# Optimization experiments

Measured on AMD Instinct MI355X. Metric: run time of the kernel, lower is better.

Reference implementation:

```python
import jax, jax.numpy as jnp
import numpy as np

N = 10000      # atoms
E = 160000     # edges (avg degree 16)
G = 20         # graphs
Z = 10         # num_elements
K = 64         # hidden scalar channels (hidden_irreps multiplicity)
NB = 8         # num_bessel
H = 64         # radial MLP width
LMAX = 3
LM = (LMAX + 1) ** 2   # 16 spherical-harmonic components
M = 16         # MLP_irreps width for final nonlinear readout
R_MAX = 5.0
AVG_NEIGH = 16.0
LS = np.array([l for l in range(LMAX + 1) for _ in range(2 * l + 1)])  # l index of each lm slot


def _sph(u):
    # real spherical harmonics up to l=3, 'component' normalization, on unit vectors u [E,3]
    x, y, z = u[:, 0], u[:, 1], u[:, 2]
    s3, s5, s15, s7 = 3.0 ** 0.5, 5.0 ** 0.5, 15.0 ** 0.5, 7.0 ** 0.5
    c31, c32, c33 = (21.0 / 8.0) ** 0.5, 105.0 ** 0.5, (35.0 / 8.0) ** 0.5
    Y = [jnp.ones_like(x),
         s3 * x, s3 * y, s3 * z,
         s15 * x * y, s15 * y * z, 0.5 * s5 * (3 * z * z - 1.0), s15 * x * z, 0.5 * s15 * (x * x - y * y),
         c33 * y * (3 * x * x - y * y), c32 * x * y * z, c31 * y * (5 * z * z - 1.0),
         0.5 * s7 * z * (5 * z * z - 3.0),
         c31 * x * (5 * z * z - 1.0), 0.5 * c32 * z * (x * x - y * y), c33 * x * (x * x - 3 * y * y)]
    return jnp.stack(Y, axis=-1)


def _radial(r):
    # Bessel radial basis with p=5 polynomial cutoff envelope
    u = r / R_MAX
    n = jnp.arange(1, NB + 1, dtype=r.dtype)
    bess = (2.0 / R_MAX) ** 0.5 * jnp.sin(n[None, :] * jnp.pi * u[:, None]) / r[:, None]
    env = jnp.where(u < 1.0, 1.0 - 21.0 * u ** 5 + 35.0 * u ** 6 - 15.0 * u ** 7, 0.0)
    return bess * env[:, None]


def _forward(node_attrs, positions, atomic_energies, W_embed, radial_W0, radial_W1, radial_W2, radial_W3, W_mix, Wz, W_out, w_read1, W_r1, w_r2, edge_index, batch):
    sender, receiver = edge_index[0], edge_index[1]
    vec = positions[receiver] - positions[sender]          # edge gather
    r = jnp.sqrt(jnp.sum(vec * vec, axis=-1) + 1e-12)
    Y = _sph(vec / r[:, None])                             # [E, 16]
    edge_feats = _radial(r)                                # [E, NB]
    node_e0 = node_attrs @ atomic_energies                 # [N]
    feats = node_attrs @ W_embed                           # node embedding [N, K]
    node_en = node_e0
    for t in range(2):  # num_interactions
        # radial MLP -> per-(channel,l) tensor-product weights
        h = edge_feats
        for W in (radial_W0[t], radial_W1[t], radial_W2[t]):
            h = jax.nn.silu(h @ W)
        Rw = (h @ radial_W3[t]).reshape(-1, K, LMAX + 1)[:, :, LS]   # [E, K, 16]
        # channelwise tensor product: sender feats x SH x radial weights
        msg = feats[sender][:, :, None] * Rw * Y[:, None, :]         # [E, K, 16]
        A = jax.ops.segment_sum(msg, receiver, num_segments=node_attrs.shape[0]) / AVG_NEIGH
        A = jnp.einsum('nkm,mkc->ncm', A, W_mix[t][LS])              # per-l linear channel mixing
        # equivariant product basis (correlation 3) -> invariant contractions with element-dep weights
        s1 = A[:, :, 0]
        inv2 = jnp.sum(A * A, axis=-1)
        b = (node_attrs @ Wz[t, 0]) * s1 + (node_attrs @ Wz[t, 1]) * inv2 + (node_attrs @ Wz[t, 2]) * (s1 * inv2)
        feats = b @ W_out[t]
        if t == 0:
            node_en = node_en + feats @ w_read1              # linear readout
        else:
            node_en = node_en + jax.nn.silu(feats @ W_r1) @ w_r2  # nonlinear readout
    return jax.ops.segment_sum(node_en, batch, num_segments=G)      # per-graph energies [G]


def setup_inputs():
    key = jax.random.key(0)
    ks = jax.random.split(key, 16)
    gn = lambda k, shape, fan: jax.random.normal(k, shape, dtype=jnp.float32) / (fan ** 0.5)
    species = jax.random.randint(ks[0], (N,), 0, Z)
    return {
        'node_attrs': jax.nn.one_hot(species, Z, dtype=jnp.float32),
        'positions': jax.random.normal(ks[1], (N, 3), dtype=jnp.float32) * 3.0,
        'edge_index': jax.random.randint(ks[2], (2, E), 0, N),
        'batch': jnp.sort(jax.random.randint(ks[3], (N,), 0, G)),
        'atomic_energies': jax.random.normal(ks[4], (Z,), dtype=jnp.float32),
        'W_embed': gn(ks[5], (Z, K), Z),
        'radial_W0': gn(ks[6], (2, NB, H), NB),
        'radial_W1': gn(ks[7], (2, H, H), H),
        'radial_W2': gn(ks[8], (2, H, H), H),
        'radial_W3': gn(ks[9], (2, H, K * (LMAX + 1)), H),
        'W_mix': gn(ks[10], (2, LMAX + 1, K, K), K),
        'Wz': gn(ks[11], (2, 3, Z, K), Z),
        'W_out': gn(ks[12], (2, K, K), K),
        'w_read1': gn(ks[13], (K,), K),
        'W_r1': gn(ks[14], (K, M), K),
        'w_r2': gn(ks[15], (M,), M),
    }


def reference(node_attrs, positions, edge_index, batch, atomic_energies, W_embed, radial_W0, radial_W1, radial_W2, radial_W3, W_mix, Wz, W_out, w_read1, W_r1, w_r2):
    return _forward(node_attrs, positions, atomic_energies, W_embed, radial_W0, radial_W1, radial_W2, radial_W3, W_mix, Wz, W_out, w_read1, W_r1, w_r2, edge_index, batch)
```

## Files before the change

kernel.cpp:

```cpp
#include <hip/hip_runtime.h>
#include <hip/hip_bf16.h>
#include <math.h>

#define NN 10000
#define NE 160000
#define NG 20
#define NZ 10
#define INV_AVG 0.0625f

typedef __attribute__((ext_vector_type(8))) short bf16x8;
typedef __attribute__((ext_vector_type(4))) float f32x4;
typedef __attribute__((ext_vector_type(4))) unsigned short u16x4;
typedef __attribute__((ext_vector_type(8))) unsigned short u16x8;

__device__ __forceinline__ float silu(float x) { return x / (1.0f + __expf(-x)); }

__device__ __forceinline__ unsigned short f2b(float f) {
    union { float f; unsigned u; } v; v.f = f;
    unsigned r = v.u + 0x7FFF + ((v.u >> 16) & 1);
    return (unsigned short)(r >> 16);
}
__device__ __forceinline__ float b2f(unsigned short h) {
    union { unsigned u; float f; } v; v.u = ((unsigned)h) << 16; return v.f;
}

__global__ __launch_bounds__(256) void node_init(
    const float* __restrict__ attrs, const float* __restrict__ W_embed,
    const float* __restrict__ ae,
    float* __restrict__ feats, float* __restrict__ node_en)
{
    int gid = blockIdx.x * blockDim.x + threadIdx.x;
    if (gid >= NN * 64) return;
    int n = gid >> 6, k = gid & 63;
    float acc = 0.f;
#pragma unroll
    for (int z = 0; z < NZ; ++z) acc += attrs[n * NZ + z] * W_embed[z * 64 + k];
    feats[gid] = acc;
    if (k == 0) {
        float e0 = 0.f;
#pragma unroll
        for (int z = 0; z < NZ; ++z) e0 += attrs[n * NZ + z] * ae[z];
        node_en[n] = e0;
    }
}

__global__ __launch_bounds__(256) void csr_count(const int* __restrict__ ei, int* __restrict__ cnt)
{
    int e = blockIdx.x * 256 + threadIdx.x;
    if (e < NE) atomicAdd(&cnt[ei[NE + e]], 1);
}

__global__ __launch_bounds__(1024) void csr_scan(const int* __restrict__ cnt, int* __restrict__ row)
{
    __shared__ int part[1024];
    const int tid = threadIdx.x;
    const int base = tid * 10;
    int loc[10];
    int s = 0;
#pragma unroll
    for (int q = 0; q < 10; ++q) {
        int idx = base + q;
        int v = (idx < NN) ? cnt[idx] : 0;
        loc[q] = s; s += v;
    }
    part[tid] = s;
    __syncthreads();
    for (int off = 1; off < 1024; off <<= 1) {
        int v = (tid >= off) ? part[tid - off] : 0;
        __syncthreads();
        part[tid] += v;
        __syncthreads();
    }
    int pre = (tid > 0) ? part[tid - 1] : 0;
#pragma unroll
    for (int q = 0; q < 10; ++q) {
        int idx = base + q;
        if (idx < NN) row[idx] = pre + loc[q];
    }
    if (tid == 1023) row[NN] = part[1023];
}

__global__ __launch_bounds__(256) void csr_scatter(
    const int* __restrict__ ei, const int* __restrict__ row,
    int* __restrict__ cur, int* __restrict__ perm)
{
    int e = blockIdx.x * 256 + threadIdx.x;
    if (e < NE) {
        int r = ei[NE + e];
        int p = atomicAdd(&cur[r], 1);
        perm[row[r] + p] = e;
    }
}

__global__ __launch_bounds__(256) void w_prep(
    const float* __restrict__ rW0, const float* __restrict__ rW1,
    const float* __restrict__ rW2, const float* __restrict__ rW3,
    const float* __restrict__ Wmix,
    unsigned short* __restrict__ w0f, unsigned short* __restrict__ w1f,
// ... 12 lines not shown
        int fidx = x >> 9, l = (x >> 3) & 63, j = x & 7;
        int kt = fidx >> 2, nt = fidx & 3;
        int k = kt * 32 + (l >> 4) * 8 + j, c = nt * 16 + (l & 15);
        w1f[x0] = f2b(rW1[t * 4096 + k * 64 + c]);
    } else if (g < 36864) {
        int x0 = g - 20480;
        int t = x0 >> 13, x = x0 & 8191;
        int fidx = x >> 9, l = (x >> 3) & 63, j = x & 7;
        int kt = fidx >> 2, nt = fidx & 3;
        int k = kt * 32 + (l >> 4) * 8 + j, c = nt * 16 + (l & 15);
        w2f[x0] = f2b(rW2[t * 4096 + k * 64 + c]);
    } else if (g < 69632) {
        int x0 = g - 36864;
        int t = x0 >> 14, x = x0 & 16383;
        int fidx = x >> 9, l = (x >> 3) & 63, j = x & 7;
        int kt = fidx >> 4, nt = fidx & 15;
        int k = kt * 32 + (l >> 4) * 8 + j, c = nt * 16 + (l & 15);
        w3f[x0] = f2b(rW3[t * 16384 + k * 256 + c]);
    } else if (g < 102400) {
        int x0 = g - 69632;
        int t = x0 >> 14;
        int x = x0 & 16383;
        int l = x >> 12;
        int xx = x & 4095;
        int f = xx >> 9, ll = (xx >> 3) & 63, j = xx & 7;
        int kt = f >> 2, ct = f & 3;
        int k = kt * 32 + (ll >> 4) * 8 + j, c = ct * 16 + (ll & 15);
        wmixf[x0] = f2b(Wmix[t * 16384 + l * 4096 + k * 64 + c]);
    }
}

__global__ __launch_bounds__(256) void edge_geom(
    const int* __restrict__ ei, const float* __restrict__ pos,
    const int* __restrict__ perm,
    unsigned short* __restrict__ ybg, unsigned short* __restrict__ ebg,
    int* __restrict__ snd_p)
{
    const int g = blockIdx.x * 256 + threadIdx.x;
    const int e = perm[g];
    const int snd = ei[e], rcv = ei[NE + e];
    snd_p[g] = snd;
    const float dx = pos[rcv * 3 + 0] - pos[snd * 3 + 0];
    const float dy = pos[rcv * 3 + 1] - pos[snd * 3 + 1];
    const float dz = pos[rcv * 3 + 2] - pos[snd * 3 + 2];
    const float r = sqrtf(dx * dx + dy * dy + dz * dz + 1e-12f);
    const float ir = 1.0f / r;
    const float x = dx * ir, y = dy * ir, z = dz * ir;
    const float xx = x * x, yy = y * y, zz = z * z;

    u16x8 ylo, yhi;
    ylo[0] = f2b(1.0f);
    ylo[1] = f2b(1.73205081f * x);
    ylo[2] = f2b(1.73205081f * y);
    ylo[3] = f2b(1.73205081f * z);
    ylo[4] = f2b(3.87298335f * x * y);
    ylo[5] = f2b(3.87298335f * y * z);
    ylo[6] = f2b(1.11803399f * (3.0f * zz - 1.0f));
    ylo[7] = f2b(3.87298335f * x * z);
    yhi[0] = f2b(1.93649167f * (xx - yy));
    yhi[1] = f2b(2.09165007f * y * (3.0f * xx - yy));
    yhi[2] = f2b(10.2469508f * x * y * z);
    yhi[3] = f2b(1.62018517f * y * (5.0f * zz - 1.0f));
    yhi[4] = f2b(1.32287566f * z * (5.0f * zz - 3.0f));
    yhi[5] = f2b(1.62018517f * x * (5.0f * zz - 1.0f));
    yhi[6] = f2b(5.12347538f * z * (xx - yy));
    yhi[7] = f2b(2.09165007f * x * (xx - 3.0f * yy));
    *(u16x8*)&ybg[(size_t)g * 16] = ylo;
    *(u16x8*)&ybg[(size_t)g * 16 + 8] = yhi;

    const float u = r * 0.2f;
    float env = 0.0f;
    if (u < 1.0f) {
        const float u2 = u * u, u5 = u2 * u2 * u;
        env = 1.0f - 21.0f * u5 + 35.0f * u5 * u - 15.0f * u5 * u2;
    }
    const float cb = 0.632455532f * ir * env;
    const float pu = 3.14159265358979f * u;
    u16x8 eb;
#pragma unroll
    for (int i = 0; i < 8; ++i) eb[i] = f2b(cb * __sinf((float)(i + 1) * pu));
    *(u16x8*)&ebg[(size_t)g * 8] = eb;
}

__global__ __launch_bounds__(256) void radial_fused(
    const unsigned short* __restrict__ ebg,
    const unsigned short* __restrict__ w0f,
    const unsigned short* __restrict__ w1f,
    const unsigned short* __restrict__ w2f,
    const unsigned short* __restrict__ w3f,
    unsigned short* __restrict__ rwb)
{
    __shared__ unsigned short sP[4][2][16 * 72];
    const int w = threadIdx.x >> 6, lane = threadIdx.x & 63;
    const int tIdx = blockIdx.x * 4 + w;
    const int lg = lane >> 4, e16 = lane & 15;
    unsigned short* ping = &sP[w][0][0];
    unsigned short* pong = &sP[w][1][0];

    const size_t g0 = (size_t)tIdx * 16;
    f32x4 c[4];

    bf16x8 a1 = {0, 0, 0, 0, 0, 0, 0, 0};
    if (lg == 0) a1 = *(const bf16x8*)&ebg[(g0 + e16) * 8];
#pragma unroll
    for (int nt = 0; nt < 4; ++nt) {
        const bf16x8 b = *(const bf16x8*)&w0f[nt * 512 + lane * 8];
        c[nt] = __builtin_amdgcn_mfma_f32_16x16x32_bf16(a1, b, (f32x4){0.f, 0.f, 0.f, 0.f}, 0, 0, 0);
    }
#pragma unroll
    for (int nt = 0; nt < 4; ++nt)
#pragma unroll
        for (int jj = 0; jj < 4; ++jj)
            ping[(lg * 4 + jj) * 72 + nt * 16 + e16] = f2b(silu(c[nt][jj]));

    {
        const bf16x8 ak0 = *(const bf16x8*)&ping[e16 * 72 + lg * 8];
        const bf16x8 ak1 = *(const bf16x8*)&ping[e16 * 72 + 32 + lg * 8];
#pragma unroll
        for (int nt = 0; nt < 4; ++nt) {
            const bf16x8 b0 = *(const bf16x8*)&w1f[nt * 512 + lane * 8];
            const bf16x8 b1 = *(const bf16x8*)&w1f[(4 + nt) * 512 + lane * 8];
            f32x4 acc = __builtin_amdgcn_mfma_f32_16x16x32_bf16(ak0, b0, (f32x4){0.f, 0.f, 0.f, 0.f}, 0, 0, 0);
            c[nt] = __builtin_amdgcn_mfma_f32_16x16x32_bf16(ak1, b1, acc, 0, 0, 0);
        }
    }
#pragma unroll
    for (int nt = 0; nt < 4; ++nt)
#pragma unroll
        for (int jj = 0; jj < 4; ++jj)
            pong[(lg * 4 + jj) * 72 + nt * 16 + e16] = f2b(silu(c[nt][jj]));

    {
        const bf16x8 ak0 = *(const bf16x8*)&pong[e16 * 72 + lg * 8];
        const bf16x8 ak1 = *(const bf16x8*)&pong[e16 * 72 + 32 + lg * 8];
#pragma unroll
        for (int nt = 0; nt < 4; ++nt) {
            const bf16x8 b0 = *(const bf16x8*)&w2f[nt * 512 + lane * 8];
            const bf16x8 b1 = *(const bf16x8*)&w2f[(4 + nt) * 512 + lane * 8];
            f32x4 acc = __builtin_amdgcn_mfma_f32_16x16x32_bf16(ak0, b0, (f32x4){0.f, 0.f, 0.f, 0.f}, 0, 0, 0);
            c[nt] = __builtin_amdgcn_mfma_f32_16x16x32_bf16(ak1, b1, acc, 0, 0, 0);
        }
    }
#pragma unroll
    for (int nt = 0; nt < 4; ++nt)
#pragma unroll
        for (int jj = 0; jj < 4; ++jj)
            ping[(lg * 4 + jj) * 72 + nt * 16 + e16] = f2b(silu(c[nt][jj]));

    const bf16x8 h0 = *(const bf16x8*)&ping[e16 * 72 + lg * 8];
    const bf16x8 h1 = *(const bf16x8*)&ping[e16 * 72 + 32 + lg * 8];
#pragma unroll 4
    for (int nt = 0; nt < 16; ++nt) {
        const bf16x8 b0 = *(const bf16x8*)&w3f[nt * 512 + lane * 8];
        const bf16x8 b1 = *(const bf16x8*)&w3f[(16 + nt) * 512 + lane * 8];
        f32x4 cc = __builtin_amdgcn_mfma_f32_16x16x32_bf16(b0, h0, (f32x4){0.f, 0.f, 0.f, 0.f}, 0, 0, 0);
        cc = __builtin_amdgcn_mfma_f32_16x16x32_bf16(b1, h1, cc, 0, 0, 0);
        u16x4 o;
#pragma unroll
        for (int jj = 0; jj < 4; ++jj) o[jj] = f2b(cc[jj]);
        *(u16x4*)&rwb[(g0 + e16) * 256 + nt * 16 + lg * 4] = o;
    }
}

#define EDGE_FMA(rv_, f_, y0_, y1_) do { \
    const float p0 = (f_) * b2f((rv_)[0]), p1 = (f_) * b2f((rv_)[1]); \
    const float p2 = (f_) * b2f((rv_)[2]), p3 = (f_) * b2f((rv_)[3]); \
    acc[0]  += p0 * b2f((y0_)[0]); \
    acc[1]  += p1 * b2f((y0_)[1]);  acc[2]  += p1 * b2f((y0_)[2]);  acc[3]  += p1 * b2f((y0_)[3]); \
    acc[4]  += p2 * b2f((y0_)[4]);  acc[5]  += p2 * b2f((y0_)[5]);  acc[6]  += p2 * b2f((y0_)[6]); \
    acc[7]  += p2 * b2f((y0_)[7]);  acc[8]  += p2 * b2f((y1_)[0]); \
    acc[9]  += p3 * b2f((y1_)[1]);  acc[10] += p3 * b2f((y1_)[2]);  acc[11] += p3 * b2f((y1_)[3]); \
    acc[12] += p3 * b2f((y1_)[4]);  acc[13] += p3 * b2f((y1_)[5]);  acc[14] += p3 * b2f((y1_)[6]); \
    acc[15] += p3 * b2f((y1_)[7]); \
} while (0)

__global__ __launch_bounds__(256) void msg_accum(
    const unsigned short* __restrict__ rwb, const unsigned short* __restrict__ ybg,
    const int* __restrict__ row, const int* __restrict__ snd_p,
    const float* __restrict__ feats_in, unsigned short* __restrict__ Abp)
{
    const int w = threadIdx.x >> 6, lane = threadIdx.x & 63;
    const int n = blockIdx.x * 4 + w;
    const int beg = row[n], end = row[n + 1];

    float acc[16];
#pragma unroll
    for (int m = 0; m < 16; ++m) acc[m] = 0.f;

    int g = beg;
    for (; g + 8 <= end; g += 8) {
        u16x4 rv[8]; float f[8]; u16x8 y0[8], y1[8];
#pragma unroll
        for (int j = 0; j < 8; ++j) {
            const int gg = g + j;
            rv[j] = *(const u16x4*)&rwb[(size_t)gg * 256 + lane * 4];
            f[j]  = feats_in[(size_t)snd_p[gg] * 64 + lane];
            y0[j] = *(const u16x8*)&ybg[(size_t)gg * 16];
            y1[j] = *(const u16x8*)&ybg[(size_t)gg * 16 + 8];
        }
#pragma unroll
        for (int j = 0; j < 8; ++j) EDGE_FMA(rv[j], f[j], y0[j], y1[j]);
    }
    for (; g < end; ++g) {
        const u16x4 rv = *(const u16x4*)&rwb[(size_t)g * 256 + lane * 4];
        const float f = feats_in[(size_t)snd_p[g] * 64 + lane];
        const u16x8 y0 = *(const u16x8*)&ybg[(size_t)g * 16];
        const u16x8 y1 = *(const u16x8*)&ybg[(size_t)g * 16 + 8];
        EDGE_FMA(rv, f, y0, y1);
    }

#pragma unroll
    for (int m = 0; m < 16; ++m)
        Abp[(size_t)m * 640000 + (size_t)n * 64 + lane] = f2b(acc[m] * INV_AVG);
}

__global__ __launch_bounds__(256) void einsum_gemm(
    const unsigned short* __restrict__ Abp,
    const unsigned short* __restrict__ wmixf,
    unsigned short* __restrict__ newb)
{
    const int w = threadIdx.x >> 6, lane = threadIdx.x & 63;
    const int lg = lane >> 4, n16 = lane & 15;
    const size_t node = (size_t)blockIdx.x * 16 + n16;

#pragma unroll
    for (int q = 0; q < 4; ++q) {
        const int m = w * 4 + q;
        const int l = (m == 0) ? 0 : (m < 4) ? 1 : (m < 9) ? 2 : 3;
        const unsigned short* Am = Abp + (size_t)m * 640000;
        const bf16x8 a0 = *(const bf16x8*)&Am[node * 64 + lg * 8];
        const bf16x8 a1 = *(const bf16x8*)&Am[node * 64 + 32 + lg * 8];
        const unsigned short* Wl = wmixf + l * 4096;
#pragma unroll
        for (int ct = 0; ct < 4; ++ct) {
            const bf16x8 b0 = *(const bf16x8*)&Wl[(0 * 4 + ct) * 512 + lane * 8];
            const bf16x8 b1 = *(const bf16x8*)&Wl[(1 * 4 + ct) * 512 + lane * 8];
            f32x4 cc = __builtin_amdgcn_mfma_f32_16x16x32_bf16(b0, a0, (f32x4){0.f, 0.f, 0.f, 0.f}, 0, 0, 0);
            cc = __builtin_amdgcn_mfma_f32_16x16x32_bf16(b1, a1, cc, 0, 0, 0);
            u16x4 o;
#pragma unroll
            for (int jj = 0; jj < 4; ++jj) o[jj] = f2b(cc[jj]);
            *(u16x4*)&newb[node * 1024 + m * 64 + ct * 16 + lg * 4] = o;
        }
    }
}

__global__ __launch_bounds__(256) void gate_update(
    const unsigned short* __restrict__ newb, const float* __restrict__ attrs,
    const float* __restrict__ Wz, const float* __restrict__ Wout,
    const float* __restrict__ wread1, const float* __restrict__ Wr1,
    const float* __restrict__ wr2,
    float* __restrict__ feats_out, float* __restrict__ node_en, int t)
{
    __shared__ float sF[4][64];
    const int w = threadIdx.x >> 6;
    const int lane = threadIdx.x & 63;
    const int n = __builtin_amdgcn_readfirstlane(blockIdx.x * 4 + w);

    float vals[16];
#pragma unroll
    for (int m = 0; m < 16; ++m)
        vals[m] = b2f(newb[(size_t)n * 1024 + m * 64 + lane]);

    const float s1 = vals[0];
    float inv2 = 0.f;
#pragma unroll
    for (int m = 0; m < 16; ++m) inv2 += vals[m] * vals[m];

    float z0 = 0.f, z1 = 0.f, z2 = 0.f;
#pragma unroll
    for (int zz = 0; zz < NZ; ++zz) {
        const float a = attrs[n * NZ + zz];
        z0 += a * Wz[(t * 3 + 0) * 640 + zz * 64 + lane];
        z1 += a * Wz[(t * 3 + 1) * 640 + zz * 64 + lane];
        z2 += a * Wz[(t * 3 + 2) * 640 + zz * 64 + lane];
    }
    const float b = z0 * s1 + z1 * inv2 + z2 * (s1 * inv2);

    sF[w][lane] = b;
    float fnew = 0.f;
#pragma unroll 8
    for (int j = 0; j < 64; ++j) fnew += sF[w][j] * Wout[j * 64 + lane];
    feats_out[(size_t)n * 64 + lane] = fnew;

    if (t == 0) {
        float v = fnew * wread1[lane];
#pragma unroll
        for (int off = 32; off > 0; off >>= 1) v += __shfl_down(v, off, 64);
        if (lane == 0) node_en[n] += v;
    } else {
        sF[w][lane] = fnew;
        if (lane < 16) {
            float a = 0.f;
#pragma unroll 8
            for (int j = 0; j < 64; ++j) a += sF[w][j] * Wr1[j * 16 + lane];
            float vv = silu(a) * wr2[lane];
            vv += __shfl_down(vv, 8, 64);
            vv += __shfl_down(vv, 4, 64);
            vv += __shfl_down(vv, 2, 64);
            vv += __shfl_down(vv, 1, 64);
            if (lane == 0) node_en[n] += vv;
        }
    }
}

__global__ __launch_bounds__(1024) void final_reduce(
    const float* __restrict__ node_en, const int* __restrict__ batch,
    float* __restrict__ out)
{
    __shared__ float sg[NG];
    if (threadIdx.x < NG) sg[threadIdx.x] = 0.f;
    __syncthreads();
    for (int n = threadIdx.x; n < NN; n += 1024)
        atomicAdd(&sg[batch[n]], node_en[n]);
    __syncthreads();
    if (threadIdx.x < NG) out[threadIdx.x] = sg[threadIdx.x];
}

extern "C" void kernel_launch(void* const* d_in, const int* in_sizes, int n_in,
                              void* d_out, int out_size, void* d_ws, size_t ws_size,
                              hipStream_t stream) {
    const float* attrs   = (const float*)d_in[0];
    const float* pos     = (const float*)d_in[1];
    const int*   ei      = (const int*)d_in[2];
    const int*   batch   = (const int*)d_in[3];
    const float* ae      = (const float*)d_in[4];
    const float* W_embed = (const float*)d_in[5];
    const float* rW0     = (const float*)d_in[6];
    const float* rW1     = (const float*)d_in[7];
    const float* rW2     = (const float*)d_in[8];
    const float* rW3     = (const float*)d_in[9];
    const float* Wmix    = (const float*)d_in[10];
    const float* Wz      = (const float*)d_in[11];
    const float* Wout    = (const float*)d_in[12];
    const float* wread1  = (const float*)d_in[13];
    const float* Wr1     = (const float*)d_in[14];
    const float* wr2     = (const float*)d_in[15];
    float* out = (float*)d_out;

    char* ws = (char*)d_ws;
    unsigned short* rwb  = (unsigned short*)(ws);
    unsigned short* newb = (unsigned short*)(ws);
    unsigned short* ybg  = (unsigned short*)(ws + 81920000);
    unsigned short* ebg  = (unsigned short*)(ws + 87040000);
    float* feats0        = (float*)(ws + 89600000);
    float* feats1        = (float*)(ws + 92160000);
    unsigned short* Abp  = (unsigned short*)(ws + 94720000);
    unsigned short* w0f  = (unsigned short*)(ws + 115200000);
    unsigned short* w1f  = (unsigned short*)(ws + 115208192);
    unsigned short* w2f  = (unsigned short*)(ws + 115240960);
    unsigned short* w3f  = (unsigned short*)(ws + 115273728);
    unsigned short* wmixf= (unsigned short*)(ws + 115339264);
    int* cnt             = (int*)(ws + 115404800);
    int* cur             = (int*)(ws + 115445760);
    int* rowst           = (int*)(ws + 115486720);
    int* perm            = (int*)(ws + 115527696);
    int* snd_p           = (int*)(ws + 116167696);
    float* node_en       = (float*)(ws + 116807696);

    hipMemsetAsync(cnt, 0, 81920, stream);

    node_init<<<2500, 256, 0, stream>>>(attrs, W_embed, ae, feats0, node_en);

    csr_count<<<625, 256, 0, stream>>>(ei, cnt);
    csr_scan<<<1, 1024, 0, stream>>>(cnt, rowst);
    csr_scatter<<<625, 256, 0, stream>>>(ei, rowst, cur, perm);

    w_prep<<<400, 256, 0, stream>>>(rW0, rW1, rW2, rW3, Wmix,
                                    w0f, w1f, w2f, w3f, wmixf);
    edge_geom<<<625, 256, 0, stream>>>(ei, pos, perm, ybg, ebg, snd_p);

    for (int t = 0; t < 2; ++t) {
        radial_fused<<<2500, 256, 0, stream>>>(
            ebg, w0f + t * 2048, w1f + t * 8192, w2f + t * 8192, w3f + t * 16384, rwb);
        msg_accum<<<2500, 256, 0, stream>>>(
            rwb, ybg, rowst, snd_p, (t == 0) ? feats0 : feats1, Abp);
        einsum_gemm<<<625, 256, 0, stream>>>(Abp, wmixf + t * 16384, newb);
        gate_update<<<2500, 256, 0, stream>>>(
            newb, attrs, Wz, Wout + t * 4096,
            wread1, Wr1, wr2,
            (t == 0) ? feats1 : feats0, node_en, t);
    }
    final_reduce<<<1, 1024, 0, stream>>>(node_en, batch, out);
}
```

Before: 289.2 us.

## Fuse radial MLP into per-node message accumulation via LDS staging

Merges the radial MLP kernel into the message accumulation kernel. Each wave now runs the MLP on 16-edge chunks of its receiver's CSR segment and stages the 256-wide radial weights in LDS instead of writing and reading back a large bf16 buffer in global memory. This removes the E×256 bf16 round trip and one launch per interaction. In exchange, a node with fewer than 16 edges still runs a full 16-row MFMA tile, so partially wasted compute on irregular degrees, and the larger LDS footprint per block may lower occupancy. Padded LDS strides are also changed.

```diff
diff --git a/kernel.cpp b/kernel.cpp
--- a/kernel.cpp
+++ b/kernel.cpp
@@ -12,6 +12,9 @@
 typedef __attribute__((ext_vector_type(4))) float f32x4;
 typedef __attribute__((ext_vector_type(4))) unsigned short u16x4;
 typedef __attribute__((ext_vector_type(8))) unsigned short u16x8;
+
+#define PSTRIDE 76
+#define RSTRIDE 260
 
 __device__ __forceinline__ float silu(float x) { return x / (1.0f + __expf(-x)); }
 
@@ -192,86 +195,6 @@
     *(u16x8*)&ebg[(size_t)g * 8] = eb;
 }
 
-__global__ __launch_bounds__(256) void radial_fused(
-    const unsigned short* __restrict__ ebg,
-    const unsigned short* __restrict__ w0f,
-    const unsigned short* __restrict__ w1f,
-    const unsigned short* __restrict__ w2f,
-    const unsigned short* __restrict__ w3f,
-    unsigned short* __restrict__ rwb)
-{
-    __shared__ unsigned short sP[4][2][16 * 72];
-    const int w = threadIdx.x >> 6, lane = threadIdx.x & 63;
-    const int tIdx = blockIdx.x * 4 + w;
-    const int lg = lane >> 4, e16 = lane & 15;
-    unsigned short* ping = &sP[w][0][0];
-    unsigned short* pong = &sP[w][1][0];
-
-    const size_t g0 = (size_t)tIdx * 16;
-    f32x4 c[4];
-
-    bf16x8 a1 = {0, 0, 0, 0, 0, 0, 0, 0};
-    if (lg == 0) a1 = *(const bf16x8*)&ebg[(g0 + e16) * 8];
-#pragma unroll
-    for (int nt = 0; nt < 4; ++nt) {
-        const bf16x8 b = *(const bf16x8*)&w0f[nt * 512 + lane * 8];
-        c[nt] = __builtin_amdgcn_mfma_f32_16x16x32_bf16(a1, b, (f32x4){0.f, 0.f, 0.f, 0.f}, 0, 0, 0);
-    }
-#pragma unroll
-    for (int nt = 0; nt < 4; ++nt)
-#pragma unroll
-        for (int jj = 0; jj < 4; ++jj)
-            ping[(lg * 4 + jj) * 72 + nt * 16 + e16] = f2b(silu(c[nt][jj]));
-
-    {
-        const bf16x8 ak0 = *(const bf16x8*)&ping[e16 * 72 + lg * 8];
-        const bf16x8 ak1 = *(const bf16x8*)&ping[e16 * 72 + 32 + lg * 8];
-#pragma unroll
-        for (int nt = 0; nt < 4; ++nt) {
-            const bf16x8 b0 = *(const bf16x8*)&w1f[nt * 512 + lane * 8];
-            const bf16x8 b1 = *(const bf16x8*)&w1f[(4 + nt) * 512 + lane * 8];
-            f32x4 acc = __builtin_amdgcn_mfma_f32_16x16x32_bf16(ak0, b0, (f32x4){0.f, 0.f, 0.f, 0.f}, 0, 0, 0);
-            c[nt] = __builtin_amdgcn_mfma_f32_16x16x32_bf16(ak1, b1, acc, 0, 0, 0);
-        }
-    }
-#pragma unroll
-    for (int nt = 0; nt < 4; ++nt)
-#pragma unroll
-        for (int jj = 0; jj < 4; ++jj)
-            pong[(lg * 4 + jj) * 72 + nt * 16 + e16] = f2b(silu(c[nt][jj]));
-
-    {
-        const bf16x8 ak0 = *(const bf16x8*)&pong[e16 * 72 + lg * 8];
-        const bf16x8 ak1 = *(const bf16x8*)&pong[e16 * 72 + 32 + lg * 8];
-#pragma unroll
-        for (int nt = 0; nt < 4; ++nt) {
-            const bf16x8 b0 = *(const bf16x8*)&w2f[nt * 512 + lane * 8];
-            const bf16x8 b1 = *(const bf16x8*)&w2f[(4 + nt) * 512 + lane * 8];
-            f32x4 acc = __builtin_amdgcn_mfma_f32_16x16x32_bf16(ak0, b0, (f32x4){0.f, 0.f, 0.f, 0.f}, 0, 0, 0);
-            c[nt] = __builtin_amdgcn_mfma_f32_16x16x32_bf16(ak1, b1, acc, 0, 0, 0);
-        }
-    }
-#pragma unroll
-    for (int nt = 0; nt < 4; ++nt)
-#pragma unroll
-        for (int jj = 0; jj < 4; ++jj)
-            ping[(lg * 4 + jj) * 72 + nt * 16 + e16] = f2b(silu(c[nt][jj]));
-
-    const bf16x8 h0 = *(const bf16x8*)&ping[e16 * 72 + lg * 8];
-    const bf16x8 h1 = *(const bf16x8*)&ping[e16 * 72 + 32 + lg * 8];
-#pragma unroll 4
-    for (int nt = 0; nt < 16; ++nt) {
-        const bf16x8 b0 = *(const bf16x8*)&w3f[nt * 512 + lane * 8];
-        const bf16x8 b1 = *(const bf16x8*)&w3f[(16 + nt) * 512 + lane * 8];
-        f32x4 cc = __builtin_amdgcn_mfma_f32_16x16x32_bf16(b0, h0, (f32x4){0.f, 0.f, 0.f, 0.f}, 0, 0, 0);
-        cc = __builtin_amdgcn_mfma_f32_16x16x32_bf16(b1, h1, cc, 0, 0, 0);
-        u16x4 o;
-#pragma unroll
-        for (int jj = 0; jj < 4; ++jj) o[jj] = f2b(cc[jj]);
-        *(u16x4*)&rwb[(g0 + e16) * 256 + nt * 16 + lg * 4] = o;
-    }
-}
-
 #define EDGE_FMA(rv_, f_, y0_, y1_) do { \
     const float p0 = (f_) * b2f((rv_)[0]), p1 = (f_) * b2f((rv_)[1]); \
     const float p2 = (f_) * b2f((rv_)[2]), p3 = (f_) * b2f((rv_)[3]); \
@@ -284,39 +207,121 @@
     acc[15] += p3 * b2f((y1_)[7]); \
 } while (0)
 
-__global__ __launch_bounds__(256) void msg_accum(
-    const unsigned short* __restrict__ rwb, const unsigned short* __restrict__ ybg,
+__global__ __launch_bounds__(256) void edge_msg_fused(
+    const unsigned short* __restrict__ ebg,
+    const unsigned short* __restrict__ ybg,
     const int* __restrict__ row, const int* __restrict__ snd_p,
-    const float* __restrict__ feats_in, unsigned short* __restrict__ Abp)
-{
+    const float* __restrict__ feats_in,
+    const unsigned short* __restrict__ w0f,
+    const unsigned short* __restrict__ w1f,
+    const unsigned short* __restrict__ w2f,
+    const unsigned short* __restrict__ w3f,
+    unsigned short* __restrict__ Abp)
+{
+    __shared__ unsigned short sP[4][2][16 * PSTRIDE];
+    __shared__ unsigned short sR[4][16 * RSTRIDE];
     const int w = threadIdx.x >> 6, lane = threadIdx.x & 63;
+    const int lg = lane >> 4, e16 = lane & 15;
     const int n = blockIdx.x * 4 + w;
     const int beg = row[n], end = row[n + 1];
+    unsigned short* ping = &sP[w][0][0];
+    unsigned short* pong = &sP[w][1][0];
+    unsigned short* sRw  = &sR[w][0];
 
     float acc[16];
 #pragma unroll
     for (int m = 0; m < 16; ++m) acc[m] = 0.f;
 
-    int g = beg;
-    for (; g + 8 <= end; g += 8) {
-        u16x4 rv[8]; float f[8]; u16x8 y0[8], y1[8];
-#pragma unroll
-        for (int j = 0; j < 8; ++j) {
-            const int gg = g + j;
-            rv[j] = *(const u16x4*)&rwb[(size_t)gg * 256 + lane * 4];
-            f[j]  = feats_in[(size_t)snd_p[gg] * 64 + lane];
-            y0[j] = *(const u16x8*)&ybg[(size_t)gg * 16];
-            y1[j] = *(const u16x8*)&ybg[(size_t)gg * 16 + 8];
-        }
-#pragma unroll
-        for (int j = 0; j < 8; ++j) EDGE_FMA(rv[j], f[j], y0[j], y1[j]);
-    }
-    for (; g < end; ++g) {
-        const u16x4 rv = *(const u16x4*)&rwb[(size_t)g * 256 + lane * 4];
-        const float f = feats_in[(size_t)snd_p[g] * 64 + lane];
-        const u16x8 y0 = *(const u16x8*)&ybg[(size_t)g * 16];
-        const u16x8 y1 = *(const u16x8*)&ybg[(size_t)g * 16 + 8];
-        EDGE_FMA(rv, f, y0, y1);
+    for (int s = beg; s < end; s += 16) {
+        const int cnt = (end - s < 16) ? (end - s) : 16;
+        const int gg = s + (e16 < cnt ? e16 : 0);
+        f32x4 c[4];
+
+        bf16x8 a1 = {0, 0, 0, 0, 0, 0, 0, 0};
+        if (lg == 0) a1 = *(const bf16x8*)&ebg[(size_t)gg * 8];
+#pragma unroll
+        for (int nt = 0; nt < 4; ++nt) {
+            const bf16x8 b = *(const bf16x8*)&w0f[nt * 512 + lane * 8];
+            c[nt] = __builtin_amdgcn_mfma_f32_16x16x32_bf16(a1, b, (f32x4){0.f, 0.f, 0.f, 0.f}, 0, 0, 0);
+        }
+#pragma unroll
+        for (int nt = 0; nt < 4; ++nt)
+#pragma unroll
+            for (int jj = 0; jj < 4; ++jj)
+                ping[(lg * 4 + jj) * PSTRIDE + nt * 16 + e16] = f2b(silu(c[nt][jj]));
+
+        {
+            const bf16x8 ak0 = *(const bf16x8*)&ping[e16 * PSTRIDE + lg * 8];
+            const bf16x8 ak1 = *(const bf16x8*)&ping[e16 * PSTRIDE + 32 + lg * 8];
+#pragma unroll
+            for (int nt = 0; nt < 4; ++nt) {
+                const bf16x8 b0 = *(const bf16x8*)&w1f[nt * 512 + lane * 8];
+                const bf16x8 b1 = *(const bf16x8*)&w1f[(4 + nt) * 512 + lane * 8];
+                f32x4 a = __builtin_amdgcn_mfma_f32_16x16x32_bf16(ak0, b0, (f32x4){0.f, 0.f, 0.f, 0.f}, 0, 0, 0);
+                c[nt] = __builtin_amdgcn_mfma_f32_16x16x32_bf16(ak1, b1, a, 0, 0, 0);
+            }
+        }
+#pragma unroll
+        for (int nt = 0; nt < 4; ++nt)
+#pragma unroll
+            for (int jj = 0; jj < 4; ++jj)
+                pong[(lg * 4 + jj) * PSTRIDE + nt * 16 + e16] = f2b(silu(c[nt][jj]));
+
+        {
+            const bf16x8 ak0 = *(const bf16x8*)&pong[e16 * PSTRIDE + lg * 8];
+            const bf16x8 ak1 = *(const bf16x8*)&pong[e16 * PSTRIDE + 32 + lg * 8];
+#pragma unroll
+            for (int nt = 0; nt < 4; ++nt) {
+                const bf16x8 b0 = *(const bf16x8*)&w2f[nt * 512 + lane * 8];
+                const bf16x8 b1 = *(const bf16x8*)&w2f[(4 + nt) * 512 + lane * 8];
+                f32x4 a = __builtin_amdgcn_mfma_f32_16x16x32_bf16(ak0, b0, (f32x4){0.f, 0.f, 0.f, 0.f}, 0, 0, 0);
+                c[nt] = __builtin_amdgcn_mfma_f32_16x16x32_bf16(ak1, b1, a, 0, 0, 0);
+            }
+        }
+#pragma unroll
+        for (int nt = 0; nt < 4; ++nt)
+#pragma unroll
+            for (int jj = 0; jj < 4; ++jj)
+                ping[(lg * 4 + jj) * PSTRIDE + nt * 16 + e16] = f2b(silu(c[nt][jj]));
+
+        {
+            const bf16x8 h0 = *(const bf16x8*)&ping[e16 * PSTRIDE + lg * 8];
+            const bf16x8 h1 = *(const bf16x8*)&ping[e16 * PSTRIDE + 32 + lg * 8];
+#pragma unroll 4
+            for (int nt = 0; nt < 16; ++nt) {
+                const bf16x8 b0 = *(const bf16x8*)&w3f[nt * 512 + lane * 8];
+                const bf16x8 b1 = *(const bf16x8*)&w3f[(16 + nt) * 512 + lane * 8];
+                f32x4 cc = __builtin_amdgcn_mfma_f32_16x16x32_bf16(b0, h0, (f32x4){0.f, 0.f, 0.f, 0.f}, 0, 0, 0);
+                cc = __builtin_amdgcn_mfma_f32_16x16x32_bf16(b1, h1, cc, 0, 0, 0);
+                u16x4 o;
+#pragma unroll
+                for (int jj = 0; jj < 4; ++jj) o[jj] = f2b(cc[jj]);
+                *(u16x4*)&sRw[e16 * RSTRIDE + nt * 16 + lg * 4] = o;
+            }
+        }
+
+        int j = 0;
+        for (; j + 8 <= cnt; j += 8) {
+            u16x4 rv[8]; float f[8]; u16x8 y0[8], y1[8];
+#pragma unroll
+            for (int q = 0; q < 8; ++q) {
+                const int g2 = s + j + q;
+                rv[q] = *(const u16x4*)&sRw[(j + q) * RSTRIDE + lane * 4];
+                f[q]  = feats_in[(size_t)snd_p[g2] * 64 + lane];
+                y0[q] = *(const u16x8*)&ybg[(size_t)g2 * 16];
+                y1[q] = *(const u16x8*)&ybg[(size_t)g2 * 16 + 8];
+            }
+#pragma unroll
+            for (int q = 0; q < 8; ++q) EDGE_FMA(rv[q], f[q], y0[q], y1[q]);
+        }
+        for (; j < cnt; ++j) {
+            const int g2 = s + j;
+            const u16x4 rv = *(const u16x4*)&sRw[j * RSTRIDE + lane * 4];
+            const float f = feats_in[(size_t)snd_p[g2] * 64 + lane];
+            const u16x8 y0 = *(const u16x8*)&ybg[(size_t)g2 * 16];
+            const u16x8 y1 = *(const u16x8*)&ybg[(size_t)g2 * 16 + 8];
+            EDGE_FMA(rv, f, y0, y1);
+        }
     }
 
 #pragma unroll
@@ -449,7 +454,6 @@
     float* out = (float*)d_out;
 
     char* ws = (char*)d_ws;
-    unsigned short* rwb  = (unsigned short*)(ws);
     unsigned short* newb = (unsigned short*)(ws);
     unsigned short* ybg  = (unsigned short*)(ws + 81920000);
     unsigned short* ebg  = (unsigned short*)(ws + 87040000);
@@ -481,10 +485,10 @@
     edge_geom<<<625, 256, 0, stream>>>(ei, pos, perm, ybg, ebg, snd_p);
 
     for (int t = 0; t < 2; ++t) {
-        radial_fused<<<2500, 256, 0, stream>>>(
-            ebg, w0f + t * 2048, w1f + t * 8192, w2f + t * 8192, w3f + t * 16384, rwb);
-        msg_accum<<<2500, 256, 0, stream>>>(
-            rwb, ybg, rowst, snd_p, (t == 0) ? feats0 : feats1, Abp);
+        edge_msg_fused<<<2500, 256, 0, stream>>>(
+            ebg, ybg, rowst, snd_p, (t == 0) ? feats0 : feats1,
+            w0f + t * 2048, w1f + t * 8192, w2f + t * 8192, w3f + t * 16384,
+            Abp);
         einsum_gemm<<<625, 256, 0, stream>>>(Abp, wmixf + t * 16384, newb);
         gate_update<<<2500, 256, 0, stream>>>(
             newb, attrs, Wz, Wout + t * 4096,
```

New measurement: 428.2 us. +48.1%, slower.

## Split node edge lists across two waves and grid-stride the radial MLP

Applied to the files above, without the earlier changes.

msg_accum now assigns two wavefronts per node, each handling half of that node's edges. Partial accumulators are combined through shared memory after a block barrier, which doubles the wave count to hide gather latency and balance degree variance. radial_fused becomes a grid-stride loop at half the grid size, so each wave processes two edge tiles, and its LDS row stride changes from 72 to 76 to alter bank mapping. The costs are an extra __syncthreads, a shared-memory reduction, and extra LDS traffic.

```diff
diff --git a/kernel.cpp b/kernel.cpp
--- a/kernel.cpp
+++ b/kernel.cpp
@@ -7,6 +7,7 @@
 #define NG 20
 #define NZ 10
 #define INV_AVG 0.0625f
+#define PSTRIDE 76
 
 typedef __attribute__((ext_vector_type(8))) short bf16x8;
 typedef __attribute__((ext_vector_type(4))) float f32x4;
@@ -200,75 +201,78 @@
     const unsigned short* __restrict__ w3f,
     unsigned short* __restrict__ rwb)
 {
-    __shared__ unsigned short sP[4][2][16 * 72];
+    __shared__ unsigned short sP[4][2][16 * PSTRIDE];
     const int w = threadIdx.x >> 6, lane = threadIdx.x & 63;
-    const int tIdx = blockIdx.x * 4 + w;
     const int lg = lane >> 4, e16 = lane & 15;
     unsigned short* ping = &sP[w][0][0];
     unsigned short* pong = &sP[w][1][0];
 
-    const size_t g0 = (size_t)tIdx * 16;
-    f32x4 c[4];
-
-    bf16x8 a1 = {0, 0, 0, 0, 0, 0, 0, 0};
-    if (lg == 0) a1 = *(const bf16x8*)&ebg[(g0 + e16) * 8];
-#pragma unroll
-    for (int nt = 0; nt < 4; ++nt) {
-        const bf16x8 b = *(const bf16x8*)&w0f[nt * 512 + lane * 8];
-        c[nt] = __builtin_amdgcn_mfma_f32_16x16x32_bf16(a1, b, (f32x4){0.f, 0.f, 0.f, 0.f}, 0, 0, 0);
-    }
-#pragma unroll
-    for (int nt = 0; nt < 4; ++nt)
-#pragma unroll
-        for (int jj = 0; jj < 4; ++jj)
-            ping[(lg * 4 + jj) * 72 + nt * 16 + e16] = f2b(silu(c[nt][jj]));
-
-    {
-        const bf16x8 ak0 = *(const bf16x8*)&ping[e16 * 72 + lg * 8];
-        const bf16x8 ak1 = *(const bf16x8*)&ping[e16 * 72 + 32 + lg * 8];
+    for (int tIdx = blockIdx.x * 4 + w; tIdx < 10000; tIdx += gridDim.x * 4) {
+        const size_t g0 = (size_t)tIdx * 16;
+        f32x4 c[4];
+
+        bf16x8 a1 = {0, 0, 0, 0, 0, 0, 0, 0};
+        if (lg == 0) a1 = *(const bf16x8*)&ebg[(g0 + e16) * 8];
 #pragma unroll
         for (int nt = 0; nt < 4; ++nt) {
-            const bf16x8 b0 = *(const bf16x8*)&w1f[nt * 512 + lane * 8];
-            const bf16x8 b1 = *(const bf16x8*)&w1f[(4 + nt) * 512 + lane * 8];
-            f32x4 acc = __builtin_amdgcn_mfma_f32_16x16x32_bf16(ak0, b0, (f32x4){0.f, 0.f, 0.f, 0.f}, 0, 0, 0);
-            c[nt] = __builtin_amdgcn_mfma_f32_16x16x32_bf16(ak1, b1, acc, 0, 0, 0);
-        }
-    }
-#pragma unroll
-    for (int nt = 0; nt < 4; ++nt)
-#pragma unroll
-        for (int jj = 0; jj < 4; ++jj)
-            pong[(lg * 4 + jj) * 72 + nt * 16 + e16] = f2b(silu(c[nt][jj]));
-
-    {
-        const bf16x8 ak0 = *(const bf16x8*)&pong[e16 * 72 + lg * 8];
-        const bf16x8 ak1 = *(const bf16x8*)&pong[e16 * 72 + 32 + lg * 8];
-#pragma unroll
-        for (int nt = 0; nt < 4; ++nt) {
-            const bf16x8 b0 = *(const bf16x8*)&w2f[nt * 512 + lane * 8];
-            const bf16x8 b1 = *(const bf16x8*)&w2f[(4 + nt) * 512 + lane * 8];
-            f32x4 acc = __builtin_amdgcn_mfma_f32_16x16x32_bf16(ak0, b0, (f32x4){0.f, 0.f, 0.f, 0.f}, 0, 0, 0);
-            c[nt] = __builtin_amdgcn_mfma_f32_16x16x32_bf16(ak1, b1, acc, 0, 0, 0);
-        }
-    }
-#pragma unroll
-    for (int nt = 0; nt < 4; ++nt)
-#pragma unroll
-        for (int jj = 0; jj < 4; ++jj)
-            ping[(lg * 4 + jj) * 72 + nt * 16 + e16] = f2b(silu(c[nt][jj]));
-
-    const bf16x8 h0 = *(const bf16x8*)&ping[e16 * 72 + lg * 8];
-    const bf16x8 h1 = *(const bf16x8*)&ping[e16 * 72 + 32 + lg * 8];
+            const bf16x8 b = *(const bf16x8*)&w0f[nt * 512 + lane * 8];
+            c[nt] = __builtin_amdgcn_mfma_f32_16x16x32_bf16(a1, b, (f32x4){0.f, 0.f, 0.f, 0.f}, 0, 0, 0);
+        }
+#pragma unroll
+        for (int nt = 0; nt < 4; ++nt)
+#pragma unroll
+            for (int jj = 0; jj < 4; ++jj)
+                ping[(lg * 4 + jj) * PSTRIDE + nt * 16 + e16] = f2b(silu(c[nt][jj]));
+
+        {
+            const bf16x8 ak0 = *(const bf16x8*)&ping[e16 * PSTRIDE + lg * 8];
+            const bf16x8 ak1 = *(const bf16x8*)&ping[e16 * PSTRIDE + 32 + lg * 8];
+#pragma unroll
+            for (int nt = 0; nt < 4; ++nt) {
+                const bf16x8 b0 = *(const bf16x8*)&w1f[nt * 512 + lane * 8];
+                const bf16x8 b1 = *(const bf16x8*)&w1f[(4 + nt) * 512 + lane * 8];
+                f32x4 acc = __builtin_amdgcn_mfma_f32_16x16x32_bf16(ak0, b0, (f32x4){0.f, 0.f, 0.f, 0.f}, 0, 0, 0);
+                c[nt] = __builtin_amdgcn_mfma_f32_16x16x32_bf16(ak1, b1, acc, 0, 0, 0);
+            }
+        }
+#pragma unroll
+        for (int nt = 0; nt < 4; ++nt)
+#pragma unroll
+            for (int jj = 0; jj < 4; ++jj)
+                pong[(lg * 4 + jj) * PSTRIDE + nt * 16 + e16] = f2b(silu(c[nt][jj]));
+
+        {
+            const bf16x8 ak0 = *(const bf16x8*)&pong[e16 * PSTRIDE + lg * 8];
+            const bf16x8 ak1 = *(const bf16x8*)&pong[e16 * PSTRIDE + 32 + lg * 8];
+#pragma unroll
+            for (int nt = 0; nt < 4; ++nt) {
+                const bf16x8 b0 = *(const bf16x8*)&w2f[nt * 512 + lane * 8];
+                const bf16x8 b1 = *(const bf16x8*)&w2f[(4 + nt) * 512 + lane * 8];
+                f32x4 acc = __builtin_amdgcn_mfma_f32_16x16x32_bf16(ak0, b0, (f32x4){0.f, 0.f, 0.f, 0.f}, 0, 0, 0);
+                c[nt] = __builtin_amdgcn_mfma_f32_16x16x32_bf16(ak1, b1, acc, 0, 0, 0);
+            }
+        }
+#pragma unroll
+        for (int nt = 0; nt < 4; ++nt)
+#pragma unroll
+            for (int jj = 0; jj < 4; ++jj)
+                ping[(lg * 4 + jj) * PSTRIDE + nt * 16 + e16] = f2b(silu(c[nt][jj]));
+
+        {
+            const bf16x8 h0 = *(const bf16x8*)&ping[e16 * PSTRIDE + lg * 8];
+            const bf16x8 h1 = *(const bf16x8*)&ping[e16 * PSTRIDE + 32 + lg * 8];
 #pragma unroll 4
-    for (int nt = 0; nt < 16; ++nt) {
-        const bf16x8 b0 = *(const bf16x8*)&w3f[nt * 512 + lane * 8];
-        const bf16x8 b1 = *(const bf16x8*)&w3f[(16 + nt) * 512 + lane * 8];
-        f32x4 cc = __builtin_amdgcn_mfma_f32_16x16x32_bf16(b0, h0, (f32x4){0.f, 0.f, 0.f, 0.f}, 0, 0, 0);
-        cc = __builtin_amdgcn_mfma_f32_16x16x32_bf16(b1, h1, cc, 0, 0, 0);
-        u16x4 o;
-#pragma unroll
-        for (int jj = 0; jj < 4; ++jj) o[jj] = f2b(cc[jj]);
-        *(u16x4*)&rwb[(g0 + e16) * 256 + nt * 16 + lg * 4] = o;
+            for (int nt = 0; nt < 16; ++nt) {
+                const bf16x8 b0 = *(const bf16x8*)&w3f[nt * 512 + lane * 8];
+                const bf16x8 b1 = *(const bf16x8*)&w3f[(16 + nt) * 512 + lane * 8];
+                f32x4 cc = __builtin_amdgcn_mfma_f32_16x16x32_bf16(b0, h0, (f32x4){0.f, 0.f, 0.f, 0.f}, 0, 0, 0);
+                cc = __builtin_amdgcn_mfma_f32_16x16x32_bf16(b1, h1, cc, 0, 0, 0);
+                u16x4 o;
+#pragma unroll
+                for (int jj = 0; jj < 4; ++jj) o[jj] = f2b(cc[jj]);
+                *(u16x4*)&rwb[(g0 + e16) * 256 + nt * 16 + lg * 4] = o;
+            }
+        }
     }
 }
 
@@ -289,9 +293,14 @@
     const int* __restrict__ row, const int* __restrict__ snd_p,
     const float* __restrict__ feats_in, unsigned short* __restrict__ Abp)
 {
+    __shared__ float sAcc[2][64 * 20];
     const int w = threadIdx.x >> 6, lane = threadIdx.x & 63;
-    const int n = blockIdx.x * 4 + w;
-    const int beg = row[n], end = row[n + 1];
+    const int nl = w >> 1, half = w & 1;
+    const int n = blockIdx.x * 2 + nl;
+    const int beg0 = row[n], end0 = row[n + 1];
+    const int h0 = (end0 - beg0 + 1) >> 1;
+    const int beg = half ? (beg0 + h0) : beg0;
+    const int end = half ? end0 : (beg0 + h0);
 
     float acc[16];
 #pragma unroll
@@ -319,9 +328,22 @@
         EDGE_FMA(rv, f, y0, y1);
     }
 
-#pragma unroll
-    for (int m = 0; m < 16; ++m)
-        Abp[(size_t)m * 640000 + (size_t)n * 64 + lane] = f2b(acc[m] * INV_AVG);
+    if (half) {
+        float4* v = (float4*)&sAcc[nl][lane * 20];
+        v[0] = make_float4(acc[0], acc[1], acc[2], acc[3]);
+        v[1] = make_float4(acc[4], acc[5], acc[6], acc[7]);
+        v[2] = make_float4(acc[8], acc[9], acc[10], acc[11]);
+        v[3] = make_float4(acc[12], acc[13], acc[14], acc[15]);
+    }
+    __syncthreads();
+    if (!half) {
+        const float* p = &sAcc[nl][lane * 20];
+#pragma unroll
+        for (int m = 0; m < 16; ++m) acc[m] += p[m];
+#pragma unroll
+        for (int m = 0; m < 16; ++m)
+            Abp[(size_t)m * 640000 + (size_t)n * 64 + lane] = f2b(acc[m] * INV_AVG);
+    }
 }
 
 __global__ __launch_bounds__(256) void einsum_gemm(
@@ -481,9 +503,9 @@
     edge_geom<<<625, 256, 0, stream>>>(ei, pos, perm, ybg, ebg, snd_p);
 
     for (int t = 0; t < 2; ++t) {
-        radial_fused<<<2500, 256, 0, stream>>>(
+        radial_fused<<<1250, 256, 0, stream>>>(
             ebg, w0f + t * 2048, w1f + t * 8192, w2f + t * 8192, w3f + t * 16384, rwb);
-        msg_accum<<<2500, 256, 0, stream>>>(
+        msg_accum<<<5000, 256, 0, stream>>>(
             rwb, ybg, rowst, snd_p, (t == 0) ? feats0 : feats1, Abp);
         einsum_gemm<<<625, 256, 0, stream>>>(Abp, wmixf + t * 16384, newb);
         gate_update<<<2500, 256, 0, stream>>>(
```

Result: no change. 291.3 us (+0.8%).

## Fuse einsum GEMM with gate update via shared memory; pad LDS stride

Applied to the files above, without the earlier changes.

Merges the channel-mixing MFMA GEMM and the gated update into one kernel. Mixed features for 16 nodes are staged in padded shared memory instead of being written to and re-read from a global bf16 buffer. The radial MLP's LDS row stride changes from 72 to 76 to reduce bank conflicts, and silu now uses a hardware reciprocal instead of a division. In exchange, each block of the fused kernel handles 16 nodes serially per wave in the gate phase, with fewer blocks and more shared memory per block, which may lower occupancy.

```diff
diff --git a/kernel.cpp b/kernel.cpp
--- a/kernel.cpp
+++ b/kernel.cpp
@@ -7,13 +7,17 @@
 #define NG 20
 #define NZ 10
 #define INV_AVG 0.0625f
+#define PSTRIDE 76
+#define NSTR 1040
 
 typedef __attribute__((ext_vector_type(8))) short bf16x8;
 typedef __attribute__((ext_vector_type(4))) float f32x4;
 typedef __attribute__((ext_vector_type(4))) unsigned short u16x4;
 typedef __attribute__((ext_vector_type(8))) unsigned short u16x8;
 
-__device__ __forceinline__ float silu(float x) { return x / (1.0f + __expf(-x)); }
+__device__ __forceinline__ float silu(float x) {
+    return x * __builtin_amdgcn_rcpf(1.0f + __expf(-x));
+}
 
 __device__ __forceinline__ unsigned short f2b(float f) {
     union { float f; unsigned u; } v; v.f = f;
@@ -200,7 +204,7 @@
     const unsigned short* __restrict__ w3f,
     unsigned short* __restrict__ rwb)
 {
-    __shared__ unsigned short sP[4][2][16 * 72];
+    __shared__ unsigned short sP[4][2][16 * PSTRIDE];
     const int w = threadIdx.x >> 6, lane = threadIdx.x & 63;
     const int tIdx = blockIdx.x * 4 + w;
     const int lg = lane >> 4, e16 = lane & 15;
@@ -221,11 +225,11 @@
     for (int nt = 0; nt < 4; ++nt)
 #pragma unroll
         for (int jj = 0; jj < 4; ++jj)
-            ping[(lg * 4 + jj) * 72 + nt * 16 + e16] = f2b(silu(c[nt][jj]));
+            ping[(lg * 4 + jj) * PSTRIDE + nt * 16 + e16] = f2b(silu(c[nt][jj]));
 
     {
-        const bf16x8 ak0 = *(const bf16x8*)&ping[e16 * 72 + lg * 8];
-        const bf16x8 ak1 = *(const bf16x8*)&ping[e16 * 72 + 32 + lg * 8];
+        const bf16x8 ak0 = *(const bf16x8*)&ping[e16 * PSTRIDE + lg * 8];
+        const bf16x8 ak1 = *(const bf16x8*)&ping[e16 * PSTRIDE + 32 + lg * 8];
 #pragma unroll
         for (int nt = 0; nt < 4; ++nt) {
             const bf16x8 b0 = *(const bf16x8*)&w1f[nt * 512 + lane * 8];
@@ -238,11 +242,11 @@
     for (int nt = 0; nt < 4; ++nt)
 #pragma unroll
         for (int jj = 0; jj < 4; ++jj)
-            pong[(lg * 4 + jj) * 72 + nt * 16 + e16] = f2b(silu(c[nt][jj]));
+            pong[(lg * 4 + jj) * PSTRIDE + nt * 16 + e16] = f2b(silu(c[nt][jj]));
 
     {
-        const bf16x8 ak0 = *(const bf16x8*)&pong[e16 * 72 + lg * 8];
-        const bf16x8 ak1 = *(const bf16x8*)&pong[e16 * 72 + 32 + lg * 8];
+        const bf16x8 ak0 = *(const bf16x8*)&pong[e16 * PSTRIDE + lg * 8];
+        const bf16x8 ak1 = *(const bf16x8*)&pong[e16 * PSTRIDE + 32 + lg * 8];
 #pragma unroll
         for (int nt = 0; nt < 4; ++nt) {
             const bf16x8 b0 = *(const bf16x8*)&w2f[nt * 512 + lane * 8];
@@ -255,20 +259,22 @@
     for (int nt = 0; nt < 4; ++nt)
 #pragma unroll
         for (int jj = 0; jj < 4; ++jj)
-            ping[(lg * 4 + jj) * 72 + nt * 16 + e16] = f2b(silu(c[nt][jj]));
-
-    const bf16x8 h0 = *(const bf16x8*)&ping[e16 * 72 + lg * 8];
-    const bf16x8 h1 = *(const bf16x8*)&ping[e16 * 72 + 32 + lg * 8];
+            ping[(lg * 4 + jj) * PSTRIDE + nt * 16 + e16] = f2b(silu(c[nt][jj]));
+
+    {
+        const bf16x8 h0 = *(const bf16x8*)&ping[e16 * PSTRIDE + lg * 8];
+        const bf16x8 h1 = *(const bf16x8*)&ping[e16 * PSTRIDE + 32 + lg * 8];
 #pragma unroll 4
-    for (int nt = 0; nt < 16; ++nt) {
-        const bf16x8 b0 = *(const bf16x8*)&w3f[nt * 512 + lane * 8];
-        const bf16x8 b1 = *(const bf16x8*)&w3f[(16 + nt) * 512 + lane * 8];
-        f32x4 cc = __builtin_amdgcn_mfma_f32_16x16x32_bf16(b0, h0, (f32x4){0.f, 0.f, 0.f, 0.f}, 0, 0, 0);
-        cc = __builtin_amdgcn_mfma_f32_16x16x32_bf16(b1, h1, cc, 0, 0, 0);
-        u16x4 o;
-#pragma unroll
-        for (int jj = 0; jj < 4; ++jj) o[jj] = f2b(cc[jj]);
-        *(u16x4*)&rwb[(g0 + e16) * 256 + nt * 16 + lg * 4] = o;
+        for (int nt = 0; nt < 16; ++nt) {
+            const bf16x8 b0 = *(const bf16x8*)&w3f[nt * 512 + lane * 8];
+            const bf16x8 b1 = *(const bf16x8*)&w3f[(16 + nt) * 512 + lane * 8];
+            f32x4 cc = __builtin_amdgcn_mfma_f32_16x16x32_bf16(b0, h0, (f32x4){0.f, 0.f, 0.f, 0.f}, 0, 0, 0);
+            cc = __builtin_amdgcn_mfma_f32_16x16x32_bf16(b1, h1, cc, 0, 0, 0);
+            u16x4 o;
+#pragma unroll
+            for (int jj = 0; jj < 4; ++jj) o[jj] = f2b(cc[jj]);
+            *(u16x4*)&rwb[(g0 + e16) * 256 + nt * 16 + lg * 4] = o;
+        }
     }
 }
 
@@ -324,92 +330,91 @@
         Abp[(size_t)m * 640000 + (size_t)n * 64 + lane] = f2b(acc[m] * INV_AVG);
 }
 
-__global__ __launch_bounds__(256) void einsum_gemm(
+__global__ __launch_bounds__(256) void einsum_gate(
     const unsigned short* __restrict__ Abp,
     const unsigned short* __restrict__ wmixf,
-    unsigned short* __restrict__ newb)
-{
+    const float* __restrict__ attrs,
+    const float* __restrict__ Wz, const float* __restrict__ Wout,
+    const float* __restrict__ wread1, const float* __restrict__ Wr1,
+    const float* __restrict__ wr2,
+    float* __restrict__ feats_out, float* __restrict__ node_en, int t)
+{
+    __shared__ unsigned short sNew[16 * NSTR];
+    __shared__ float sF[4][64];
     const int w = threadIdx.x >> 6, lane = threadIdx.x & 63;
     const int lg = lane >> 4, n16 = lane & 15;
-    const size_t node = (size_t)blockIdx.x * 16 + n16;
+    const size_t node0 = (size_t)blockIdx.x * 16;
 
 #pragma unroll
     for (int q = 0; q < 4; ++q) {
         const int m = w * 4 + q;
         const int l = (m == 0) ? 0 : (m < 4) ? 1 : (m < 9) ? 2 : 3;
         const unsigned short* Am = Abp + (size_t)m * 640000;
-        const bf16x8 a0 = *(const bf16x8*)&Am[node * 64 + lg * 8];
-        const bf16x8 a1 = *(const bf16x8*)&Am[node * 64 + 32 + lg * 8];
+        const bf16x8 a0 = *(const bf16x8*)&Am[(node0 + n16) * 64 + lg * 8];
+        const bf16x8 a1 = *(const bf16x8*)&Am[(node0 + n16) * 64 + 32 + lg * 8];
         const unsigned short* Wl = wmixf + l * 4096;
 #pragma unroll
         for (int ct = 0; ct < 4; ++ct) {
-            const bf16x8 b0 = *(const bf16x8*)&Wl[(0 * 4 + ct) * 512 + lane * 8];
-            const bf16x8 b1 = *(const bf16x8*)&Wl[(1 * 4 + ct) * 512 + lane * 8];
+            const bf16x8 b0 = *(const bf16x8*)&Wl[ct * 512 + lane * 8];
+            const bf16x8 b1 = *(const bf16x8*)&Wl[(4 + ct) * 512 + lane * 8];
             f32x4 cc = __builtin_amdgcn_mfma_f32_16x16x32_bf16(b0, a0, (f32x4){0.f, 0.f, 0.f, 0.f}, 0, 0, 0);
             cc = __builtin_amdgcn_mfma_f32_16x16x32_bf16(b1, a1, cc, 0, 0, 0);
             u16x4 o;
 #pragma unroll
             for (int jj = 0; jj < 4; ++jj) o[jj] = f2b(cc[jj]);
-            *(u16x4*)&newb[node * 1024 + m * 64 + ct * 16 + lg * 4] = o;
-        }
-    }
-}
-
-__global__ __launch_bounds__(256) void gate_update(
-    const unsigned short* __restrict__ newb, const float* __restrict__ attrs,
-    const float* __restrict__ Wz, const float* __restrict__ Wout,
-    const float* __restrict__ wread1, const float* __restrict__ Wr1,
-    const float* __restrict__ wr2,
-    float* __restrict__ feats_out, float* __restrict__ node_en, int t)
-{
-    __shared__ float sF[4][64];
-    const int w = threadIdx.x >> 6;
-    const int lane = threadIdx.x & 63;
-    const int n = __builtin_amdgcn_readfirstlane(blockIdx.x * 4 + w);
-
-    float vals[16];
-#pragma unroll
-    for (int m = 0; m < 16; ++m)
-        vals[m] = b2f(newb[(size_t)n * 1024 + m * 64 + lane]);
-
-    const float s1 = vals[0];
-    float inv2 = 0.f;
-#pragma unroll
-    for (int m = 0; m < 16; ++m) inv2 += vals[m] * vals[m];
-
-    float z0 = 0.f, z1 = 0.f, z2 = 0.f;
-#pragma unroll
-    for (int zz = 0; zz < NZ; ++zz) {
-        const float a = attrs[n * NZ + zz];
-        z0 += a * Wz[(t * 3 + 0) * 640 + zz * 64 + lane];
-        z1 += a * Wz[(t * 3 + 1) * 640 + zz * 64 + lane];
-        z2 += a * Wz[(t * 3 + 2) * 640 + zz * 64 + lane];
-    }
-    const float b = z0 * s1 + z1 * inv2 + z2 * (s1 * inv2);
-
-    sF[w][lane] = b;
-    float fnew = 0.f;
+            *(u16x4*)&sNew[n16 * NSTR + m * 64 + ct * 16 + lg * 4] = o;
+        }
+    }
+    __syncthreads();
+
+    for (int qq = 0; qq < 4; ++qq) {
+        const int nl = w * 4 + qq;
+        const int n = (int)node0 + nl;
+
+        float vals[16];
+#pragma unroll
+        for (int m = 0; m < 16; ++m)
+            vals[m] = b2f(sNew[nl * NSTR + m * 64 + lane]);
+
+        const float s1 = vals[0];
+        float inv2 = 0.f;
+#pragma unroll
+        for (int m = 0; m < 16; ++m) inv2 += vals[m] * vals[m];
+
+        float z0 = 0.f, z1 = 0.f, z2 = 0.f;
+#pragma unroll
+        for (int zz = 0; zz < NZ; ++zz) {
+            const float a = attrs[n * NZ + zz];
+            z0 += a * Wz[(t * 3 + 0) * 640 + zz * 64 + lane];
+            z1 += a * Wz[(t * 3 + 1) * 640 + zz * 64 + lane];
+            z2 += a * Wz[(t * 3 + 2) * 640 + zz * 64 + lane];
+        }
+        const float b = z0 * s1 + z1 * inv2 + z2 * (s1 * inv2);
+
+        sF[w][lane] = b;
+        float fnew = 0.f;
 #pragma unroll 8
-    for (int j = 0; j < 64; ++j) fnew += sF[w][j] * Wout[j * 64 + lane];
-    feats_out[(size_t)n * 64 + lane] = fnew;
-
-    if (t == 0) {
-        float v = fnew * wread1[lane];
-#pragma unroll
-        for (int off = 32; off > 0; off >>= 1) v += __shfl_down(v, off, 64);
-        if (lane == 0) node_en[n] += v;
-    } else {
-        sF[w][lane] = fnew;
-        if (lane < 16) {
-            float a = 0.f;
+        for (int j = 0; j < 64; ++j) fnew += sF[w][j] * Wout[j * 64 + lane];
+        feats_out[(size_t)n * 64 + lane] = fnew;
+
+        if (t == 0) {
+            float v = fnew * wread1[lane];
+#pragma unroll
+            for (int off = 32; off > 0; off >>= 1) v += __shfl_down(v, off, 64);
+            if (lane == 0) node_en[n] += v;
+        } else {
+            sF[w][lane] = fnew;
+            if (lane < 16) {
+                float a = 0.f;
 #pragma unroll 8
-            for (int j = 0; j < 64; ++j) a += sF[w][j] * Wr1[j * 16 + lane];
-            float vv = silu(a) * wr2[lane];
-            vv += __shfl_down(vv, 8, 64);
-            vv += __shfl_down(vv, 4, 64);
-            vv += __shfl_down(vv, 2, 64);
-            vv += __shfl_down(vv, 1, 64);
-            if (lane == 0) node_en[n] += vv;
+                for (int j = 0; j < 64; ++j) a += sF[w][j] * Wr1[j * 16 + lane];
+                float vv = silu(a) * wr2[lane];
+                vv += __shfl_down(vv, 8, 64);
+                vv += __shfl_down(vv, 4, 64);
+                vv += __shfl_down(vv, 2, 64);
+                vv += __shfl_down(vv, 1, 64);
+                if (lane == 0) node_en[n] += vv;
+            }
         }
     }
 }
@@ -450,7 +455,6 @@
 
     char* ws = (char*)d_ws;
     unsigned short* rwb  = (unsigned short*)(ws);
-    unsigned short* newb = (unsigned short*)(ws);
     unsigned short* ybg  = (unsigned short*)(ws + 81920000);
     unsigned short* ebg  = (unsigned short*)(ws + 87040000);
     float* feats0        = (float*)(ws + 89600000);
@@ -485,9 +489,8 @@
             ebg, w0f + t * 2048, w1f + t * 8192, w2f + t * 8192, w3f + t * 16384, rwb);
         msg_accum<<<2500, 256, 0, stream>>>(
             rwb, ybg, rowst, snd_p, (t == 0) ? feats0 : feats1, Abp);
-        einsum_gemm<<<625, 256, 0, stream>>>(Abp, wmixf + t * 16384, newb);
-        gate_update<<<2500, 256, 0, stream>>>(
-            newb, attrs, Wz, Wout + t * 4096,
+        einsum_gate<<<625, 256, 0, stream>>>(
+            Abp, wmixf + t * 16384, attrs, Wz, Wout + t * 4096,
             wread1, Wr1, wr2,
             (t == 0) ? feats1 : feats0, node_en, t);
     }
```

After: 275.3 us. 4.8% less time.
